# Kernel tuning notes

Measured on AMD Instinct MI355X. Metric: run time of the kernel, lower is better.

## Reference

```python
import jax, jax.numpy as jnp
import numpy as np

IOTA = 1.0 / 137.0
PHI = 0.618033988749894
N_SAMPLE = 5
N_SYM = 2048
HIDDEN = 2048
N_LIN_IN = 3
N_LIN_OUT = 9
EPS = 1e-9


def _instance_norm(x):
    # InstanceNorm1d, affine=False, unbatched (C, L): per-row mean/biased-var over last dim
    m = jnp.mean(x, axis=-1, keepdims=True)
    v = jnp.mean((x - m) ** 2, axis=-1, keepdims=True)
    return (x - m) * jax.lax.rsqrt(v + EPS)


def _lstm_cell(x, W_ih, W_hh, b_ih, b_hh):
    # torch.nn.LSTMCell with h0 = c0 = 0: the W_hh recurrent term is identically zero,
    # and f*c0 vanishes. Gate order (torch): i, f, g, o.
    gates = x @ W_ih.T + b_ih + b_hh  # [B, 4*HIDDEN]
    i, f, g, o = jnp.split(gates, 4, axis=-1)
    c = jax.nn.sigmoid(i) * jnp.tanh(g)
    return jax.nn.sigmoid(o) * jnp.tanh(c)


def setup_inputs() -> dict:
    key = jax.random.key(0)
    ks = jax.random.split(key, 10)
    s = 0.02
    return dict(
        signal=jax.random.normal(ks[0], (N_SAMPLE, N_SYM), jnp.float32),
        u1=jax.random.uniform(ks[1], (N_LIN_OUT, N_SYM), jnp.float32),
        u2=jax.random.uniform(ks[2], (N_LIN_OUT, HIDDEN), jnp.float32),
        bil_W=jax.random.normal(ks[3], (N_LIN_OUT, N_LIN_IN, N_LIN_IN), jnp.float32) * s,
        bil_b=jnp.zeros((N_LIN_OUT,), jnp.float32),
        Wih1=jax.random.normal(ks[4], (4 * HIDDEN, N_SYM), jnp.float32) * s,
        Whh1=jax.random.normal(ks[5], (4 * HIDDEN, HIDDEN), jnp.float32) * s,
        bih1=jnp.zeros((4 * HIDDEN,), jnp.float32),
        bhh1=jnp.zeros((4 * HIDDEN,), jnp.float32),
        Wih2=jax.random.normal(ks[6], (4 * HIDDEN, HIDDEN), jnp.float32) * s,
        Whh2=jax.random.normal(ks[7], (4 * HIDDEN, HIDDEN), jnp.float32) * s,
        bih2=jnp.zeros((4 * HIDDEN,), jnp.float32),
        bhh2=jnp.zeros((4 * HIDDEN,), jnp.float32),
        lin_W=jax.random.normal(ks[8], (N_SAMPLE * N_SYM, HIDDEN), jnp.float32) * s,
        lin_b=jnp.zeros((N_SAMPLE * N_SYM,), jnp.float32),
    )


def reference(signal, u1, u2, bil_W, bil_b, Wih1, Whh1, bih1, bhh1,
              Wih2, Whh2, bih2, bhh2, lin_W, lin_b):
    x = _instance_norm(signal.T)                    # [N_SYM, 5]
    fr = jnp.fft.rfft(x, axis=-1)                   # [N_SYM, 3] complex64
    b = jnp.nan_to_num(fr.real * fr.imag, nan=IOTA, posinf=1.0, neginf=IOTA)
    b = jax.nn.softmax(jax.nn.sigmoid(b), axis=1)   # [N_SYM, 3]
    # nn.Bilinear: out[n,k] = x1[n,i] W[k,i,j] x2[n,j] + b[k]
    b = jnp.einsum('ni,kij,nj->nk', b, bil_W, b) + bil_b  # [N_SYM, 9]
    b = IOTA + b.T * (u1 < PHI).astype(b.dtype)     # stochastic mask -> [9, N_SYM]
    h = _lstm_cell(b, Wih1, Whh1, bih1, bhh1)       # [9, HIDDEN]
    h = IOTA + h * (u2 < PHI).astype(h.dtype)
    h = _lstm_cell(h, Wih2, Whh2, bih2, bhh2)       # [9, HIDDEN]
    out = (h @ lin_W.T + lin_b).reshape(N_SAMPLE, N_SYM, N_LIN_OUT)  # view([5, N_SYM, 9])
    out = jax.nn.softmax(_instance_norm(out.sum(2)), axis=1)         # [5, N_SYM]
    return out
```

## Files before the change

### kernel.cpp

```cpp
#include <hip/hip_runtime.h>
#include <math.h>

#define IOTA_F (1.0f / 137.0f)
#define PHI_F  0.618033988749894f

__device__ __forceinline__ float sigm(float x) { return 1.0f / (1.0f + expf(-x)); }

__device__ __forceinline__ float nan2num(float v) {
    if (isnan(v)) return IOTA_F;
    if (isinf(v)) return v > 0.0f ? 1.0f : IOTA_F;
    return v;
}

__global__ void k_pre(const float* __restrict__ signal,
                      const float* __restrict__ u1,
                      const float* __restrict__ bilW,
                      const float* __restrict__ bilb,
                      float* __restrict__ B1)
{
    int s = blockIdx.x * blockDim.x + threadIdx.x;
    if (s >= 2048) return;

    float x0 = signal[0 * 2048 + s];
    float x1 = signal[1 * 2048 + s];
    float x2 = signal[2 * 2048 + s];
    float x3 = signal[3 * 2048 + s];
    float x4 = signal[4 * 2048 + s];

    float mean = (x0 + x1 + x2 + x3 + x4) * 0.2f;
    float d0 = x0 - mean, d1 = x1 - mean, d2 = x2 - mean, d3 = x3 - mean, d4 = x4 - mean;
    float var = (d0 * d0 + d1 * d1 + d2 * d2 + d3 * d3 + d4 * d4) * 0.2f;
    float r = 1.0f / sqrtf(var + 1e-9f);
    d0 *= r; d1 *= r; d2 *= r; d3 *= r; d4 *= r;

    const float c1 = 0.30901699437494742f;
    const float c2 = -0.80901699437494745f;
    const float s1 = 0.95105651629515357f;
    const float s2 = 0.58778525229247314f;

    float re1 = d0 + c1 * (d1 + d4) + c2 * (d2 + d3);
    float im1 = -(s1 * (d1 - d4) + s2 * (d2 - d3));
    float re2 = d0 + c2 * (d1 + d4) + c1 * (d2 + d3);
    float im2 = -s2 * (d1 - d4) + s1 * (d2 - d3);

    float p1 = nan2num(re1 * im1);
    float p2 = nan2num(re2 * im2);
    float g0 = 0.5f;
    float g1 = sigm(p1);
    float g2 = sigm(p2);

    float mx = fmaxf(g0, fmaxf(g1, g2));
    float e0 = expf(g0 - mx), e1 = expf(g1 - mx), e2 = expf(g2 - mx);
    float inv = 1.0f / (e0 + e1 + e2);
    float w[3] = { e0 * inv, e1 * inv, e2 * inv };

    #pragma unroll
    for (int kk = 0; kk < 9; ++kk) {
        float acc = bilb[kk];
        #pragma unroll
        for (int i = 0; i < 3; ++i)
            #pragma unroll
            for (int j = 0; j < 3; ++j)
                acc += w[i] * bilW[kk * 9 + i * 3 + j] * w[j];
        float mask = (u1[kk * 2048 + s] < PHI_F) ? 1.0f : 0.0f;
        B1[kk * 2048 + s] = IOTA_F + acc * mask;
    }
}

template <bool GATEMAP>
__global__ __launch_bounds__(256) void k_gemv9v3(
    const float* __restrict__ Bv,
    const float* __restrict__ W,
    const float* __restrict__ bias1,
    const float* __restrict__ bias2,
    float* __restrict__ Out,
    int nvrows)
{
    __shared__ float lds[4][16][9];

    const int tid  = threadIdx.x;
    const int w    = tid >> 6;
    const int lane = tid & 63;
    const int grp  = lane >> 4;
    const int li   = lane & 15;

    const int jj0 = blockIdx.x * 16;
    int jbase = jj0;
    if (GATEMAP && jj0 >= 2048) jbase += 2048;

    const float4* __restrict__ B4 = reinterpret_cast<const float4*>(Bv);
    const float4* __restrict__ W0 =
        reinterpret_cast<const float4*>(W) + ((size_t)jbase + grp * 4) * 512;

    float acc[4][9];
    #pragma unroll
    for (int r = 0; r < 4; ++r)
        #pragma unroll
        for (int m = 0; m < 9; ++m) acc[r][m] = 0.0f;

    const int kb4 = w * 128;

    #pragma unroll 2
    for (int it = 0; it < 8; ++it) {
        const int idx = kb4 + it * 16 + li;
        float4 bv[9];
        #pragma unroll
        for (int m = 0; m < 9; ++m) bv[m] = B4[m * 512 + idx];
        #pragma unroll
        for (int r = 0; r < 4; ++r) {
            float4 wv = W0[(size_t)r * 512 + idx];
            #pragma unroll
            for (int m = 0; m < 9; ++m) {
                acc[r][m] = fmaf(wv.x, bv[m].x, acc[r][m]);
                acc[r][m] = fmaf(wv.y, bv[m].y, acc[r][m]);
                acc[r][m] = fmaf(wv.z, bv[m].z, acc[r][m]);
                acc[r][m] = fmaf(wv.w, bv[m].w, acc[r][m]);
            }
        }
    }

    #pragma unroll
    for (int r = 0; r < 4; ++r)
        #pragma unroll
        for (int m = 0; m < 9; ++m) {
            float v = acc[r][m];
            v += __shfl_xor(v, 1);
            v += __shfl_xor(v, 2);
            v += __shfl_xor(v, 4);
            v += __shfl_xor(v, 8);
            acc[r][m] = v;
        }

    if (li == 0) {
        #pragma unroll
        for (int r = 0; r < 4; ++r)
            #pragma unroll
            for (int m = 0; m < 9; ++m)
                lds[w][grp * 4 + r][m] = acc[r][m];
    }
    __syncthreads();

    if (tid < 144) {
        const int row = tid / 9;
        const int m   = tid - row * 9;
        float v = lds[0][row][m] + lds[1][row][m] + lds[2][row][m] + lds[3][row][m];
        const int jj = jj0 + row;
        int j = jj;
        if (GATEMAP && jj >= 2048) j += 2048;
        if (bias1) v += bias1[j];
        if (bias2) v += bias2[j];
        Out[(size_t)m * nvrows + jj] = v;
    }
}

__global__ void k_combine(const float* __restrict__ G,
                          const float* __restrict__ u,
                          float* __restrict__ Bout)
{
    int idx = blockIdx.x * blockDim.x + threadIdx.x;
    if (idx >= 9 * 2048) return;
    int m = idx >> 11;
    int q = idx & 2047;
    const float* Gm = G + (size_t)m * 6144;
    float iv = Gm[q];
    float gv = Gm[2048 + q];
    float ov = Gm[4096 + q];
    float c = sigm(iv) * tanhf(gv);
    float h = sigm(ov) * tanhf(c);
    if (u) h = IOTA_F + h * ((u[idx] < PHI_F) ? 1.0f : 0.0f);
    Bout[idx] = h;
}

__device__ __forceinline__ float block_reduce(float v, float* red, int tid, int op) {
    #pragma unroll
    for (int off = 32; off > 0; off >>= 1) {
        float o = __shfl_xor(v, off);
        v = op ? fmaxf(v, o) : (v + o);
    }
    __syncthreads();
    if ((tid & 63) == 0) red[tid >> 6] = v;
    __syncthreads();
    float r = red[0];
    #pragma unroll
    for (int w = 1; w < 8; ++w) r = op ? fmaxf(r, red[w]) : (r + red[w]);
    return r;
}

__global__ void k_final(const float* __restrict__ Z,
                        float* __restrict__ out)
{
    __shared__ float t[2048];
    __shared__ float red[8];
    const int a = blockIdx.x;
    const int tid = threadIdx.x;

    for (int s = tid; s < 2048; s += 512) {
        const float* zp = Z + a * 18432 + s * 9;
        float acc = 0.0f;
        #pragma unroll
        for (int k = 0; k < 9; ++k) acc += zp[k];
        t[s] = acc;
    }
    __syncthreads();

    float l0 = t[tid], l1 = t[tid + 512], l2 = t[tid + 1024], l3 = t[tid + 1536];

    float ssum = block_reduce(l0 + l1 + l2 + l3, red, tid, 0);
    float mean = ssum * (1.0f / 2048.0f);
    float e0 = l0 - mean, e1 = l1 - mean, e2 = l2 - mean, e3 = l3 - mean;
    float vsum = block_reduce(e0 * e0 + e1 * e1 + e2 * e2 + e3 * e3, red, tid, 0);
    float rstd = 1.0f / sqrtf(vsum * (1.0f / 2048.0f) + 1e-9f);
    float xn0 = e0 * rstd, xn1 = e1 * rstd, xn2 = e2 * rstd, xn3 = e3 * rstd;

    float mx = block_reduce(fmaxf(fmaxf(xn0, xn1), fmaxf(xn2, xn3)), red, tid, 1);
    float ex0 = expf(xn0 - mx), ex1 = expf(xn1 - mx), ex2 = expf(xn2 - mx), ex3 = expf(xn3 - mx);
    float esum = block_reduce(ex0 + ex1 + ex2 + ex3, red, tid, 0);
    float inv = 1.0f / esum;

    out[a * 2048 + tid]        = ex0 * inv;
    out[a * 2048 + tid + 512]  = ex1 * inv;
    out[a * 2048 + tid + 1024] = ex2 * inv;
    out[a * 2048 + tid + 1536] = ex3 * inv;
}

extern "C" void kernel_launch(void* const* d_in, const int* in_sizes, int n_in,
                              void* d_out, int out_size, void* d_ws, size_t ws_size,
                              hipStream_t stream)
{
    const float* signal = (const float*)d_in[0];
    const float* u1     = (const float*)d_in[1];
    const float* u2     = (const float*)d_in[2];
    const float* bilW   = (const float*)d_in[3];
    const float* bilb   = (const float*)d_in[4];
    const float* Wih1   = (const float*)d_in[5];
    const float* bih1   = (const float*)d_in[7];
    const float* bhh1   = (const float*)d_in[8];
    const float* Wih2   = (const float*)d_in[9];
    const float* bih2   = (const float*)d_in[11];
    const float* bhh2   = (const float*)d_in[12];
    const float* linW   = (const float*)d_in[13];
    const float* linb   = (const float*)d_in[14];

    float* out = (float*)d_out;
    float* ws  = (float*)d_ws;

    float* B1 = ws;
    float* G  = ws + 18432;
    float* B2 = ws + 73728;
    float* B3 = B1;
    float* Z  = ws + 92160;

    k_pre<<<8, 256, 0, stream>>>(signal, u1, bilW, bilb, B1);

    k_gemv9v3<true><<<6144 / 16, 256, 0, stream>>>(B1, Wih1, bih1, bhh1, G, 6144);
    k_combine<<<72, 256, 0, stream>>>(G, u2, B2);

    k_gemv9v3<true><<<6144 / 16, 256, 0, stream>>>(B2, Wih2, bih2, bhh2, G, 6144);
    k_combine<<<72, 256, 0, stream>>>(G, nullptr, B3);

    k_gemv9v3<false><<<10240 / 16, 256, 0, stream>>>(B3, linW, linb, nullptr, Z, 10240);

    k_final<<<5, 512, 0, stream>>>(Z, out);
}
```

Measured before the change: 62.05 us.

## Fuse LSTM gate GEMV with cell activation and retile final linear GEMV

Each block now computes the i, g and o gate rows for four hidden units and applies the LSTM cell nonlinearity, bias and mask in-block. This removes the separate combine kernels and the intermediate gate buffer round-trip. The final linear GEMV is templated on rows-per-group (5), so it launches 512 blocks instead of 640. Fewer launches and less global traffic come at the cost of three strided weight streams per group.

```diff
diff --git a/kernel.cpp b/kernel.cpp
--- a/kernel.cpp
+++ b/kernel.cpp
@@ -67,16 +67,16 @@
     }
 }
 
-template <bool GATEMAP>
-__global__ __launch_bounds__(256) void k_gemv9v3(
+template <bool MASK>
+__global__ __launch_bounds__(256) void k_lstm_fused(
     const float* __restrict__ Bv,
     const float* __restrict__ W,
-    const float* __restrict__ bias1,
-    const float* __restrict__ bias2,
-    float* __restrict__ Out,
-    int nvrows)
-{
-    __shared__ float lds[4][16][9];
+    const float* __restrict__ b1,
+    const float* __restrict__ b2,
+    const float* __restrict__ u,
+    float* __restrict__ Bout)
+{
+    __shared__ float lds[4][4][3][9];
 
     const int tid  = threadIdx.x;
     const int w    = tid >> 6;
@@ -84,17 +84,16 @@
     const int grp  = lane >> 4;
     const int li   = lane & 15;
 
-    const int jj0 = blockIdx.x * 16;
-    int jbase = jj0;
-    if (GATEMAP && jj0 >= 2048) jbase += 2048;
+    const int q = blockIdx.x * 4 + grp;
 
     const float4* __restrict__ B4 = reinterpret_cast<const float4*>(Bv);
-    const float4* __restrict__ W0 =
-        reinterpret_cast<const float4*>(W) + ((size_t)jbase + grp * 4) * 512;
-
-    float acc[4][9];
-    #pragma unroll
-    for (int r = 0; r < 4; ++r)
+    const float4* __restrict__ Wi = reinterpret_cast<const float4*>(W) + (size_t)q * 512;
+    const float4* __restrict__ Wg = Wi + (size_t)4096 * 512;
+    const float4* __restrict__ Wo = Wi + (size_t)6144 * 512;
+
+    float acc[3][9];
+    #pragma unroll
+    for (int r = 0; r < 3; ++r)
         #pragma unroll
         for (int m = 0; m < 9; ++m) acc[r][m] = 0.0f;
 
@@ -106,8 +105,102 @@
         float4 bv[9];
         #pragma unroll
         for (int m = 0; m < 9; ++m) bv[m] = B4[m * 512 + idx];
-        #pragma unroll
-        for (int r = 0; r < 4; ++r) {
+        float4 wv0 = Wi[idx];
+        float4 wv1 = Wg[idx];
+        float4 wv2 = Wo[idx];
+        #pragma unroll
+        for (int m = 0; m < 9; ++m) {
+            acc[0][m] = fmaf(wv0.x, bv[m].x, acc[0][m]);
+            acc[0][m] = fmaf(wv0.y, bv[m].y, acc[0][m]);
+            acc[0][m] = fmaf(wv0.z, bv[m].z, acc[0][m]);
+            acc[0][m] = fmaf(wv0.w, bv[m].w, acc[0][m]);
+            acc[1][m] = fmaf(wv1.x, bv[m].x, acc[1][m]);
+            acc[1][m] = fmaf(wv1.y, bv[m].y, acc[1][m]);
+            acc[1][m] = fmaf(wv1.z, bv[m].z, acc[1][m]);
+            acc[1][m] = fmaf(wv1.w, bv[m].w, acc[1][m]);
+            acc[2][m] = fmaf(wv2.x, bv[m].x, acc[2][m]);
+            acc[2][m] = fmaf(wv2.y, bv[m].y, acc[2][m]);
+            acc[2][m] = fmaf(wv2.z, bv[m].z, acc[2][m]);
+            acc[2][m] = fmaf(wv2.w, bv[m].w, acc[2][m]);
+        }
+    }
+
+    #pragma unroll
+    for (int r = 0; r < 3; ++r)
+        #pragma unroll
+        for (int m = 0; m < 9; ++m) {
+            float v = acc[r][m];
+            v += __shfl_xor(v, 1);
+            v += __shfl_xor(v, 2);
+            v += __shfl_xor(v, 4);
+            v += __shfl_xor(v, 8);
+            acc[r][m] = v;
+        }
+
+    if (li == 0) {
+        #pragma unroll
+        for (int r = 0; r < 3; ++r)
+            #pragma unroll
+            for (int m = 0; m < 9; ++m)
+                lds[w][grp][r][m] = acc[r][m];
+    }
+    __syncthreads();
+
+    if (tid < 36) {
+        const int qq = tid / 9;
+        const int m  = tid - qq * 9;
+        const int qg = blockIdx.x * 4 + qq;
+        float iv = lds[0][qq][0][m] + lds[1][qq][0][m] + lds[2][qq][0][m] + lds[3][qq][0][m];
+        float gv = lds[0][qq][1][m] + lds[1][qq][1][m] + lds[2][qq][1][m] + lds[3][qq][1][m];
+        float ov = lds[0][qq][2][m] + lds[1][qq][2][m] + lds[2][qq][2][m] + lds[3][qq][2][m];
+        iv += b1[qg] + b2[qg];
+        gv += b1[4096 + qg] + b2[4096 + qg];
+        ov += b1[6144 + qg] + b2[6144 + qg];
+        float c = sigm(iv) * tanhf(gv);
+        float h = sigm(ov) * tanhf(c);
+        if (MASK) h = IOTA_F + h * ((u[m * 2048 + qg] < PHI_F) ? 1.0f : 0.0f);
+        Bout[m * 2048 + qg] = h;
+    }
+}
+
+template <int R>
+__global__ __launch_bounds__(256) void k_gemvR(
+    const float* __restrict__ Bv,
+    const float* __restrict__ W,
+    const float* __restrict__ bias,
+    float* __restrict__ Out,
+    int nrows)
+{
+    __shared__ float lds[4][4 * R][9];
+
+    const int tid  = threadIdx.x;
+    const int w    = tid >> 6;
+    const int lane = tid & 63;
+    const int grp  = lane >> 4;
+    const int li   = lane & 15;
+
+    const int rowB = blockIdx.x * 4 * R;
+    const int row0 = rowB + grp * R;
+
+    const float4* __restrict__ B4 = reinterpret_cast<const float4*>(Bv);
+    const float4* __restrict__ W0 = reinterpret_cast<const float4*>(W) + (size_t)row0 * 512;
+
+    float acc[R][9];
+    #pragma unroll
+    for (int r = 0; r < R; ++r)
+        #pragma unroll
+        for (int m = 0; m < 9; ++m) acc[r][m] = 0.0f;
+
+    const int kb4 = w * 128;
+
+    #pragma unroll 2
+    for (int it = 0; it < 8; ++it) {
+        const int idx = kb4 + it * 16 + li;
+        float4 bv[9];
+        #pragma unroll
+        for (int m = 0; m < 9; ++m) bv[m] = B4[m * 512 + idx];
+        #pragma unroll
+        for (int r = 0; r < R; ++r) {
             float4 wv = W0[(size_t)r * 512 + idx];
             #pragma unroll
             for (int m = 0; m < 9; ++m) {
@@ -120,7 +213,7 @@
     }
 
     #pragma unroll
-    for (int r = 0; r < 4; ++r)
+    for (int r = 0; r < R; ++r)
         #pragma unroll
         for (int m = 0; m < 9; ++m) {
             float v = acc[r][m];
@@ -133,42 +226,20 @@
 
     if (li == 0) {
         #pragma unroll
-        for (int r = 0; r < 4; ++r)
+        for (int r = 0; r < R; ++r)
             #pragma unroll
             for (int m = 0; m < 9; ++m)
-                lds[w][grp * 4 + r][m] = acc[r][m];
-    }
-    __syncthreads();
-
-    if (tid < 144) {
-        const int row = tid / 9;
-        const int m   = tid - row * 9;
+                lds[w][grp * R + r][m] = acc[r][m];
+    }
+    __syncthreads();
+
+    for (int t = tid; t < 4 * R * 9; t += 256) {
+        const int row = t / 9;
+        const int m   = t - row * 9;
         float v = lds[0][row][m] + lds[1][row][m] + lds[2][row][m] + lds[3][row][m];
-        const int jj = jj0 + row;
-        int j = jj;
-        if (GATEMAP && jj >= 2048) j += 2048;
-        if (bias1) v += bias1[j];
-        if (bias2) v += bias2[j];
-        Out[(size_t)m * nvrows + jj] = v;
-    }
-}
-
-__global__ void k_combine(const float* __restrict__ G,
-                          const float* __restrict__ u,
-                          float* __restrict__ Bout)
-{
-    int idx = blockIdx.x * blockDim.x + threadIdx.x;
-    if (idx >= 9 * 2048) return;
-    int m = idx >> 11;
-    int q = idx & 2047;
-    const float* Gm = G + (size_t)m * 6144;
-    float iv = Gm[q];
-    float gv = Gm[2048 + q];
-    float ov = Gm[4096 + q];
-    float c = sigm(iv) * tanhf(gv);
-    float h = sigm(ov) * tanhf(c);
-    if (u) h = IOTA_F + h * ((u[idx] < PHI_F) ? 1.0f : 0.0f);
-    Bout[idx] = h;
+        const int grow = rowB + row;
+        Out[(size_t)m * nrows + grow] = v + bias[grow];
+    }
 }
 
 __device__ __forceinline__ float block_reduce(float v, float* red, int tid, int op) {
@@ -245,20 +316,16 @@
     float* ws  = (float*)d_ws;
 
     float* B1 = ws;
-    float* G  = ws + 18432;
-    float* B2 = ws + 73728;
+    float* B2 = ws + 18432;
     float* B3 = B1;
-    float* Z  = ws + 92160;
+    float* Z  = ws + 36864;
 
     k_pre<<<8, 256, 0, stream>>>(signal, u1, bilW, bilb, B1);
 
-    k_gemv9v3<true><<<6144 / 16, 256, 0, stream>>>(B1, Wih1, bih1, bhh1, G, 6144);
-    k_combine<<<72, 256, 0, stream>>>(G, u2, B2);
-
-    k_gemv9v3<true><<<6144 / 16, 256, 0, stream>>>(B2, Wih2, bih2, bhh2, G, 6144);
-    k_combine<<<72, 256, 0, stream>>>(G, nullptr, B3);
-
-    k_gemv9v3<false><<<10240 / 16, 256, 0, stream>>>(B3, linW, linb, nullptr, Z, 10240);
+    k_lstm_fused<true><<<512, 256, 0, stream>>>(B1, Wih1, bih1, bhh1, u2, B2);
+    k_lstm_fused<false><<<512, 256, 0, stream>>>(B2, Wih2, bih2, bhh2, nullptr, B3);
+
+    k_gemvR<5><<<512, 256, 0, stream>>>(B3, linW, linb, Z, 10240);
 
     k_final<<<5, 512, 0, stream>>>(Z, out);
 }
```

New measurement: 56.06 us. -9.6%, faster.
